# Optimization experiments

Hardware: AMD Instinct MI355X
Metric: run time of the kernel (lower is better)

## Reference

```python
import jax, jax.numpy as jnp
import numpy as np
from jax.ops import segment_sum


def gcn_conv(x, src, dst, W, b, num_nodes):
    # PyG GCNConv: x' = D^{-1/2} (A + I) D^{-1/2} (x @ W) + b
    loops = jnp.arange(num_nodes, dtype=src.dtype)
    s = jnp.concatenate([src, loops])  # source of each edge (incl. self-loops)
    d = jnp.concatenate([dst, loops])  # destination of each edge
    ones = jnp.ones(s.shape[0], dtype=x.dtype)
    deg = segment_sum(ones, d, num_segments=num_nodes)  # in-degree incl. self-loop
    dinv = jnp.where(deg > 0, jax.lax.rsqrt(deg), 0.0)
    norm = dinv[s] * dinv[d]  # [E+N]
    h = x @ W  # [N, C_out] dense transform first (C_out <= C_in typical)
    msg = h[s] * norm[:, None]  # gather + scale  [E+N, C_out]
    out = segment_sum(msg, d, num_segments=num_nodes)  # scatter-add
    return out + b


def setup_inputs() -> dict:
    key = jax.random.key(0)
    k1, k2, k3, k4 = jax.random.split(key, 4)
    N, E = 100000, 1600000
    C_in, C_out = 64, 32
    C_hid = 2 * C_out
    x = jax.random.normal(k1, (N, C_in), dtype=jnp.float32)
    edge_index = jax.random.randint(k2, (2, E), 0, N, dtype=jnp.int64)
    # Glorot-style init for the linear weights, zero bias (PyG defaults)
    W1 = jax.random.normal(k3, (C_in, C_hid), dtype=jnp.float32) * (1.0 / np.sqrt(C_in))
    b1 = jnp.zeros((C_hid,), dtype=jnp.float32)
    W2 = jax.random.normal(k4, (C_hid, C_out), dtype=jnp.float32) * (1.0 / np.sqrt(C_hid))
    b2 = jnp.zeros((C_out,), dtype=jnp.float32)
    return {"x": x, "edge_index": edge_index, "num_nodes": N,
            "W1": W1, "b1": b1, "W2": W2, "b2": b2}


def reference(x, edge_index, num_nodes, W1, b1, W2, b2):
    src, dst = edge_index[0], edge_index[1]
    h = gcn_conv(x, src, dst, W1, b1, num_nodes)
    h = jax.nn.relu(h)
    out = gcn_conv(h, src, dst, W2, b2, num_nodes)
    return out
```

## Files before the change

kernel.cpp:

```cpp
#include <hip/hip_runtime.h>


constexpr int CAP = 4096;
constexpr int NBMAX = 1024;
constexpr float QS = 2048.f;
constexpr float QSI = 1.f / 2048.f;

__device__ inline int sxlo(unsigned u) { return (int)(short)(u & 0xffffu); }
__device__ inline int sxhi(unsigned u) { return ((int)u) >> 16; }

__global__ __launch_bounds__(256) void p1_bin(const int* __restrict__ src,
                                              const int* __restrict__ dst,
                                              int* __restrict__ bucketCursor,
                                              unsigned* __restrict__ staging, int E, int NB) {
    __shared__ int cnt[NBMAX];
    __shared__ int cur[NBMAX];
    int tid = threadIdx.x;
    for (int i = tid; i < NB; i += 256) cnt[i] = 0;
    __syncthreads();
    int e0 = blockIdx.x * 4096;
#pragma unroll
    for (int k = 0; k < 16; ++k) {
        int e = e0 + k * 256 + tid;
        if (e < E) atomicAdd(&cnt[dst[e] >> 7], 1);
    }
    __syncthreads();
    for (int i = tid; i < NB; i += 256) {
        int c = cnt[i];
        cur[i] = c ? atomicAdd(&bucketCursor[i], c) : 0;
    }
    __syncthreads();
#pragma unroll
    for (int k = 0; k < 16; ++k) {
        int e = e0 + k * 256 + tid;
        if (e < E) {
            int d = dst[e];
            int b = d >> 7;
            int slot = atomicAdd(&cur[b], 1);
            staging[(size_t)b * CAP + slot] = ((unsigned)src[e] << 7) | (unsigned)(d & 127);
        }
    }
}

__global__ __launch_bounds__(256) void deg_dinv(const unsigned* __restrict__ staging,
                                                const int* __restrict__ bucketCursor,
                                                float* __restrict__ dinv, int N) {
    __shared__ int deg[128];
    int b = blockIdx.x, tid = threadIdx.x;
    if (tid < 128) deg[tid] = 0;
    __syncthreads();
    int size = bucketCursor[b];
    const unsigned* st = staging + (size_t)b * CAP;
    for (int i = tid; i < size; i += 256) atomicAdd(&deg[st[i] & 127u], 1);
    __syncthreads();
    int g = b * 128 + tid;
    if (tid < 128 && g < N) dinv[g] = rsqrtf((float)(deg[tid] + 1));
}

__global__ __launch_bounds__(256) void gemm1(const float* __restrict__ X,
                                             const float* __restrict__ W,
                                             const float* __restrict__ dinv,
                                             unsigned* __restrict__ Hout, int N) {
    constexpr int XS = 65;
    __shared__ float Xs[128 * XS];
    __shared__ float Ws[64 * 64];
    int tid = threadIdx.x;
    int rowBase = blockIdx.x * 128;
    const float4* Wv = (const float4*)W;
    float4* Wsv = (float4*)Ws;
    for (int i = tid; i < 64 * 64 / 4; i += 256) Wsv[i] = Wv[i];
    const float4* Xv = (const float4*)X;
    for (int v = tid; v < 128 * 16; v += 256) {
        int r = v >> 4, j = v & 15;
        int gr = rowBase + r;
        float4 t = make_float4(0.f, 0.f, 0.f, 0.f);
        if (gr < N) t = Xv[(size_t)gr * 16 + j];
        int b = r * XS + j * 4;
        Xs[b] = t.x;
        Xs[b + 1] = t.y;
        Xs[b + 2] = t.z;
        Xs[b + 3] = t.w;
    }
    __syncthreads();
    int cg = tid % 8, rg = tid / 8;
    int c0 = cg * 8, r0 = rg * 4;
    float acc[4][8];
#pragma unroll
    for (int i = 0; i < 4; ++i)
#pragma unroll
        for (int j = 0; j < 8; ++j) acc[i][j] = 0.f;
#pragma unroll 8
    for (int k = 0; k < 64; ++k) {
        float4 w0 = *(const float4*)&Ws[k * 64 + c0];
        float4 w1 = *(const float4*)&Ws[k * 64 + c0 + 4];
        float xr[4];
#pragma unroll
        for (int i = 0; i < 4; ++i) xr[i] = Xs[(r0 + i) * XS + k];
#pragma unroll
        for (int i = 0; i < 4; ++i) {
            acc[i][0] = fmaf(xr[i], w0.x, acc[i][0]);
            acc[i][1] = fmaf(xr[i], w0.y, acc[i][1]);
            acc[i][2] = fmaf(xr[i], w0.z, acc[i][2]);
            acc[i][3] = fmaf(xr[i], w0.w, acc[i][3]);
            acc[i][4] = fmaf(xr[i], w1.x, acc[i][4]);
            acc[i][5] = fmaf(xr[i], w1.y, acc[i][5]);
            acc[i][6] = fmaf(xr[i], w1.z, acc[i][6]);
            acc[i][7] = fmaf(xr[i], w1.w, acc[i][7]);
        }
    }
#pragma unroll
    for (int i = 0; i < 4; ++i) {
        int row = rowBase + r0 + i;
        if (row >= N) continue;
        float dq = dinv[row] * QS;
        unsigned pk[4];
#pragma unroll
        for (int j = 0; j < 4; ++j) {
            int lo = (int)(acc[i][2 * j] * dq);
            int hi = (int)(acc[i][2 * j + 1] * dq);
            pk[j] = ((unsigned)lo & 0xffffu) | ((unsigned)hi << 16);
        }
        *(uint4*)(Hout + (size_t)row * 32 + c0 / 2) = make_uint4(pk[0], pk[1], pk[2], pk[3]);
    }
}

__global__ __launch_bounds__(256) void agg1(const uint4* __restrict__ hs1,
                                            const unsigned* __restrict__ staging,
                                            const int* __restrict__ bucketCursor,
                                            const float* __restrict__ dinv,
                                            const float* __restrict__ b1,
                                            unsigned* __restrict__ a1, int N) {
    constexpr int S1 = 65;
    __shared__ int acc[128 * S1];
    __shared__ float b1s[64];
    int b = blockIdx.x, tid = threadIdx.x;
    int gbase = b * 128;
    if (tid < 64) b1s[tid] = QS * b1[tid];
    for (int v = tid; v < 128 * 8; v += 256) {
        int n = v >> 3, j = v & 7;
        int s0 = 0, s1 = 0, s2 = 0, s3 = 0, s4 = 0, s5 = 0, s6 = 0, s7 = 0;
        if (gbase + n < N) {
            uint4 u = hs1[(size_t)(gbase + n) * 8 + j];
            s0 = sxlo(u.x); s1 = sxhi(u.x);
            s2 = sxlo(u.y); s3 = sxhi(u.y);
            s4 = sxlo(u.z); s5 = sxhi(u.z);
            s6 = sxlo(u.w); s7 = sxhi(u.w);
        }
        int* dp = &acc[n * S1 + j * 8];
        dp[0] = s0; dp[1] = s1; dp[2] = s2; dp[3] = s3;
        dp[4] = s4; dp[5] = s5; dp[6] = s6; dp[7] = s7;
    }
    __syncthreads();
    int size = bucketCursor[b];
    const unsigned* st = staging + (size_t)b * CAP;
    int g = tid >> 3, q = tid & 7;
#define ADD8(NN, U)                          \
    {                                        \
        int* ap = &acc[(int)(NN) * S1 + q * 8]; \
        atomicAdd(ap + 0, sxlo((U).x));      \
        atomicAdd(ap + 1, sxhi((U).x));      \
        atomicAdd(ap + 2, sxlo((U).y));      \
        atomicAdd(ap + 3, sxhi((U).y));      \
        atomicAdd(ap + 4, sxlo((U).z));      \
        atomicAdd(ap + 5, sxhi((U).z));      \
        atomicAdd(ap + 6, sxlo((U).w));      \
        atomicAdd(ap + 7, sxhi((U).w));      \
    }
    int i = g;
    for (; i + 224 < size; i += 256) {
        unsigned w[8];
        uint4 u[8];
#pragma unroll
        for (int k = 0; k < 8; ++k) w[k] = st[i + 32 * k];
#pragma unroll
        for (int k = 0; k < 8; ++k) u[k] = hs1[(size_t)(w[k] >> 7) * 8 + q];
#pragma unroll
        for (int k = 0; k < 8; ++k) ADD8(w[k] & 127u, u[k])
    }
    for (; i < size; i += 32) {
        unsigned w = st[i];
        uint4 u = hs1[(size_t)(w >> 7) * 8 + q];
        ADD8(w & 127u, u)
    }
#undef ADD8
    __syncthreads();
    for (int v = tid; v < 128 * 32; v += 256) {
        int n = v >> 5, cc = (v & 31) * 2;
        int gn = gbase + n;
        if (gn >= N) continue;
        float dn = dinv[gn];
        float x0 = fmaxf(fmaf((float)acc[n * S1 + cc], dn, b1s[cc]), 0.f);
        float x1 = fmaxf(fmaf((float)acc[n * S1 + cc + 1], dn, b1s[cc + 1]), 0.f);
        int q0 = (int)x0, q1 = (int)x1;
        a1[(size_t)gn * 32 + (cc >> 1)] = ((unsigned)q0 & 0xffffu) | ((unsigned)q1 << 16);
    }
}

__global__ __launch_bounds__(256) void gemm2(const uint4* __restrict__ a1,
                                             const float* __restrict__ W2,
                                             const float* __restrict__ dinv,
                                             unsigned* __restrict__ h2, int N) {
    constexpr int XS = 65;
    __shared__ float Xs[128 * XS];
    __shared__ float Ws[64 * 32];
    int tid = threadIdx.x;
    int rowBase = blockIdx.x * 128;
    const float4* Wv = (const float4*)W2;
    float4* Wsv = (float4*)Ws;
    for (int i = tid; i < 64 * 32 / 4; i += 256) Wsv[i] = Wv[i];
    for (int v = tid; v < 128 * 8; v += 256) {
        int r = v >> 3, j = v & 7;
        int gr = rowBase + r;
        float f0 = 0.f, f1 = 0.f, f2 = 0.f, f3 = 0.f, f4 = 0.f, f5 = 0.f, f6 = 0.f, f7 = 0.f;
        if (gr < N) {
            uint4 u = a1[(size_t)gr * 8 + j];
            f0 = (float)sxlo(u.x); f1 = (float)sxhi(u.x);
            f2 = (float)sxlo(u.y); f3 = (float)sxhi(u.y);
            f4 = (float)sxlo(u.z); f5 = (float)sxhi(u.z);
            f6 = (float)sxlo(u.w); f7 = (float)sxhi(u.w);
        }
        float* dp = &Xs[r * XS + j * 8];
        dp[0] = f0; dp[1] = f1; dp[2] = f2; dp[3] = f3;
        dp[4] = f4; dp[5] = f5; dp[6] = f6; dp[7] = f7;
    }
    __syncthreads();
    int cg = tid & 3, rg = tid >> 2;
    int c0 = cg * 8, r0 = rg * 2;
    float acc[2][8];
#pragma unroll
    for (int i = 0; i < 2; ++i)
#pragma unroll
        for (int j = 0; j < 8; ++j) acc[i][j] = 0.f;
#pragma unroll 8
    for (int k = 0; k < 64; ++k) {
        float4 w0 = *(const float4*)&Ws[k * 32 + c0];
        float4 w1 = *(const float4*)&Ws[k * 32 + c0 + 4];
        float x0 = Xs[r0 * XS + k];
        float x1 = Xs[(r0 + 1) * XS + k];
        acc[0][0] = fmaf(x0, w0.x, acc[0][0]);
        acc[0][1] = fmaf(x0, w0.y, acc[0][1]);
        acc[0][2] = fmaf(x0, w0.z, acc[0][2]);
        acc[0][3] = fmaf(x0, w0.w, acc[0][3]);
        acc[0][4] = fmaf(x0, w1.x, acc[0][4]);
        acc[0][5] = fmaf(x0, w1.y, acc[0][5]);
        acc[0][6] = fmaf(x0, w1.z, acc[0][6]);
        acc[0][7] = fmaf(x0, w1.w, acc[0][7]);
        acc[1][0] = fmaf(x1, w0.x, acc[1][0]);
        acc[1][1] = fmaf(x1, w0.y, acc[1][1]);
        acc[1][2] = fmaf(x1, w0.z, acc[1][2]);
        acc[1][3] = fmaf(x1, w0.w, acc[1][3]);
        acc[1][4] = fmaf(x1, w1.x, acc[1][4]);
        acc[1][5] = fmaf(x1, w1.y, acc[1][5]);
        acc[1][6] = fmaf(x1, w1.z, acc[1][6]);
        acc[1][7] = fmaf(x1, w1.w, acc[1][7]);
    }
#pragma unroll
    for (int i = 0; i < 2; ++i) {
        int row = rowBase + r0 + i;
        if (row >= N) continue;
        float dn = dinv[row];
        unsigned pk[2];
#pragma unroll
        for (int j = 0; j < 2; ++j) {
            int lo = (int)(acc[i][4 * j + 0] * dn);
            int l1 = (int)(acc[i][4 * j + 1] * dn);
            int l2 = (int)(acc[i][4 * j + 2] * dn);
            int l3 = (int)(acc[i][4 * j + 3] * dn);
            pk[0] = ((unsigned)lo & 0xffffu) | ((unsigned)l1 << 16);
            pk[1] = ((unsigned)l2 & 0xffffu) | ((unsigned)l3 << 16);
            *(uint2*)(h2 + (size_t)row * 16 + (c0 + 4 * j) / 2) = make_uint2(pk[0], pk[1]);
        }
    }
}

__global__ __launch_bounds__(256) void agg2(const uint4* __restrict__ hs2,
                                            const unsigned* __restrict__ staging,
                                            const int* __restrict__ bucketCursor,
                                            const float* __restrict__ dinv,
                                            const float* __restrict__ b2,
                                            float* __restrict__ out, int N) {
    constexpr int S2 = 33;
    __shared__ int acc[128 * S2];
    __shared__ float b2s[32];
    int b = blockIdx.x, tid = threadIdx.x;
    int gbase = b * 128;
    if (tid < 32) b2s[tid] = b2[tid];
    for (int v = tid; v < 128 * 4; v += 256) {
        int n = v >> 2, j = v & 3;
        int s0 = 0, s1 = 0, s2 = 0, s3 = 0, s4 = 0, s5 = 0, s6 = 0, s7 = 0;
        if (gbase + n < N) {
            uint4 u = hs2[(size_t)(gbase + n) * 4 + j];
            s0 = sxlo(u.x); s1 = sxhi(u.x);
            s2 = sxlo(u.y); s3 = sxhi(u.y);
            s4 = sxlo(u.z); s5 = sxhi(u.z);
            s6 = sxlo(u.w); s7 = sxhi(u.w);
        }
        int* dp = &acc[n * S2 + j * 8];
        dp[0] = s0; dp[1] = s1; dp[2] = s2; dp[3] = s3;
        dp[4] = s4; dp[5] = s5; dp[6] = s6; dp[7] = s7;
    }
    __syncthreads();
    int size = bucketCursor[b];
    const unsigned* st = staging + (size_t)b * CAP;
    int g = tid >> 2, q = tid & 3;
#define ADD8(NN, U)                          \
    {                                        \
        int* ap = &acc[(int)(NN) * S2 + q * 8]; \
        atomicAdd(ap + 0, sxlo((U).x));      \
        atomicAdd(ap + 1, sxhi((U).x));      \
        atomicAdd(ap + 2, sxlo((U).y));      \
        atomicAdd(ap + 3, sxhi((U).y));      \
        atomicAdd(ap + 4, sxlo((U).z));      \
        atomicAdd(ap + 5, sxhi((U).z));      \
        atomicAdd(ap + 6, sxlo((U).w));      \
        atomicAdd(ap + 7, sxhi((U).w));      \
    }
    int i = g;
    for (; i + 448 < size; i += 512) {
        unsigned w[8];
        uint4 u[8];
#pragma unroll
        for (int k = 0; k < 8; ++k) w[k] = st[i + 64 * k];
#pragma unroll
        for (int k = 0; k < 8; ++k) u[k] = hs2[(size_t)(w[k] >> 7) * 4 + q];
#pragma unroll
        for (int k = 0; k < 8; ++k) ADD8(w[k] & 127u, u[k])
    }
    for (; i < size; i += 64) {
        unsigned w = st[i];
        uint4 u = hs2[(size_t)(w >> 7) * 4 + q];
        ADD8(w & 127u, u)
    }
#undef ADD8
    __syncthreads();
    for (int v = tid; v < 128 * 32; v += 256) {
        int n = v >> 5, c = v & 31;
        int gn = gbase + n;
        if (gn >= N) continue;
        out[(size_t)gn * 32 + c] = fmaf((float)acc[n * S2 + c], dinv[gn] * QSI, b2s[c]);
    }
}

extern "C" void kernel_launch(void* const* d_in, const int* in_sizes, int n_in,
                              void* d_out, int out_size, void* d_ws, size_t ws_size,
                              hipStream_t stream) {
    const float* x = (const float*)d_in[0];
    const int* ei = (const int*)d_in[1];
    const float* W1 = (const float*)d_in[3];
    const float* b1 = (const float*)d_in[4];
    const float* W2 = (const float*)d_in[5];
    const float* b2 = (const float*)d_in[6];

    constexpr int CIN = 64, CHID = 64, COUT = 32;
    const int N = in_sizes[0] / CIN;
    const int E = in_sizes[1] / 2;
    const int* src = ei;
    const int* dst = ei + E;
    const int NB = (N + 127) >> 7;

    char* p = (char*)d_ws;
    auto carve = [&](size_t bytes) -> void* {
        void* q = (void*)p;
        p += (bytes + 255) & ~(size_t)255;
        return q;
    };
    int* bucketCursor = (int*)carve((size_t)NB * 4);
    float* dinv = (float*)carve((size_t)N * 4);
    unsigned* staging = (unsigned*)carve((size_t)NB * CAP * 4);
    unsigned* h1 = (unsigned*)carve((size_t)N * CHID * 2);
    unsigned* a1 = (unsigned*)carve((size_t)N * CHID * 2);
    unsigned* h2 = (unsigned*)carve((size_t)N * COUT * 2);

    hipMemsetAsync(bucketCursor, 0, (size_t)NB * 4, stream);
    p1_bin<<<(E + 4095) / 4096, 256, 0, stream>>>(src, dst, bucketCursor, staging, E, NB);
    deg_dinv<<<NB, 256, 0, stream>>>(staging, bucketCursor, dinv, N);
    gemm1<<<(N + 127) / 128, 256, 0, stream>>>(x, W1, dinv, h1, N);
    agg1<<<NB, 256, 0, stream>>>((const uint4*)h1, staging, bucketCursor, dinv, b1, a1, N);
    gemm2<<<(N + 127) / 128, 256, 0, stream>>>((const uint4*)a1, W2, dinv, h2, N);
    agg2<<<NB, 256, 0, stream>>>((const uint4*)h2, staging, bucketCursor, dinv, b2,
                                 (float*)d_out, N);
}
```

Before: 218.1 us.

## Fuse degree count into binning and gemm2 into layer-1 aggregation

Degree counting moves into the binning kernel through global atomics on a per-node int array, so the separate deg_dinv kernel is removed and consumers compute rsqrt on the fly. The layer-1 aggregation kernel now applies bias and ReLU in shared memory and runs the 64x32 second GEMM directly, which drops the a1 intermediate round trip and a launch. The binning block size is halved to 2048 edges. In exchange this adds 1.6M global atomics on deg and more shared memory per aggregation block, which may lower occupancy. It also changes numerics, because the hidden activations no longer go through int16 quantization before the second GEMM.

```diff
diff --git a/kernel.cpp b/kernel.cpp
--- a/kernel.cpp
+++ b/kernel.cpp
@@ -12,17 +12,22 @@
 __global__ __launch_bounds__(256) void p1_bin(const int* __restrict__ src,
                                               const int* __restrict__ dst,
                                               int* __restrict__ bucketCursor,
+                                              int* __restrict__ deg,
                                               unsigned* __restrict__ staging, int E, int NB) {
     __shared__ int cnt[NBMAX];
     __shared__ int cur[NBMAX];
     int tid = threadIdx.x;
     for (int i = tid; i < NB; i += 256) cnt[i] = 0;
     __syncthreads();
-    int e0 = blockIdx.x * 4096;
-#pragma unroll
-    for (int k = 0; k < 16; ++k) {
+    int e0 = blockIdx.x * 2048;
+#pragma unroll
+    for (int k = 0; k < 8; ++k) {
         int e = e0 + k * 256 + tid;
-        if (e < E) atomicAdd(&cnt[dst[e] >> 7], 1);
+        if (e < E) {
+            int d = dst[e];
+            atomicAdd(&cnt[d >> 7], 1);
+            atomicAdd(&deg[d], 1);
+        }
     }
     __syncthreads();
     for (int i = tid; i < NB; i += 256) {
@@ -31,7 +36,7 @@
     }
     __syncthreads();
 #pragma unroll
-    for (int k = 0; k < 16; ++k) {
+    for (int k = 0; k < 8; ++k) {
         int e = e0 + k * 256 + tid;
         if (e < E) {
             int d = dst[e];
@@ -42,24 +47,9 @@
     }
 }
 
-__global__ __launch_bounds__(256) void deg_dinv(const unsigned* __restrict__ staging,
-                                                const int* __restrict__ bucketCursor,
-                                                float* __restrict__ dinv, int N) {
-    __shared__ int deg[128];
-    int b = blockIdx.x, tid = threadIdx.x;
-    if (tid < 128) deg[tid] = 0;
-    __syncthreads();
-    int size = bucketCursor[b];
-    const unsigned* st = staging + (size_t)b * CAP;
-    for (int i = tid; i < size; i += 256) atomicAdd(&deg[st[i] & 127u], 1);
-    __syncthreads();
-    int g = b * 128 + tid;
-    if (tid < 128 && g < N) dinv[g] = rsqrtf((float)(deg[tid] + 1));
-}
-
 __global__ __launch_bounds__(256) void gemm1(const float* __restrict__ X,
                                              const float* __restrict__ W,
-                                             const float* __restrict__ dinv,
+                                             const int* __restrict__ deg,
                                              unsigned* __restrict__ Hout, int N) {
     constexpr int XS = 65;
     __shared__ float Xs[128 * XS];
@@ -112,7 +102,7 @@
     for (int i = 0; i < 4; ++i) {
         int row = rowBase + r0 + i;
         if (row >= N) continue;
-        float dq = dinv[row] * QS;
+        float dq = rsqrtf((float)(deg[row] + 1)) * QS;
         unsigned pk[4];
 #pragma unroll
         for (int j = 0; j < 4; ++j) {
@@ -124,18 +114,26 @@
     }
 }
 
-__global__ __launch_bounds__(256) void agg1(const uint4* __restrict__ hs1,
-                                            const unsigned* __restrict__ staging,
-                                            const int* __restrict__ bucketCursor,
-                                            const float* __restrict__ dinv,
-                                            const float* __restrict__ b1,
-                                            unsigned* __restrict__ a1, int N) {
+__global__ __launch_bounds__(256) void agg1_gemm2(
+    const uint4* __restrict__ hs1, const unsigned* __restrict__ staging,
+    const int* __restrict__ bucketCursor, const int* __restrict__ deg,
+    const float* __restrict__ b1, const float* __restrict__ W2,
+    unsigned* __restrict__ h2, int N) {
     constexpr int S1 = 65;
     __shared__ int acc[128 * S1];
+    __shared__ float Ws[64 * 32];
     __shared__ float b1s[64];
+    __shared__ float dns[128];
     int b = blockIdx.x, tid = threadIdx.x;
     int gbase = b * 128;
+    const float4* Wv = (const float4*)W2;
+    float4* Wsv = (float4*)Ws;
+    for (int i = tid; i < 64 * 32 / 4; i += 256) Wsv[i] = Wv[i];
     if (tid < 64) b1s[tid] = QS * b1[tid];
+    if (tid < 128) {
+        int gn = gbase + tid;
+        dns[tid] = (gn < N) ? rsqrtf((float)(deg[gn] + 1)) : 0.f;
+    }
     for (int v = tid; v < 128 * 8; v += 256) {
         int n = v >> 3, j = v & 7;
         int s0 = 0, s1 = 0, s2 = 0, s3 = 0, s4 = 0, s5 = 0, s6 = 0, s7 = 0;
@@ -154,17 +152,17 @@
     int size = bucketCursor[b];
     const unsigned* st = staging + (size_t)b * CAP;
     int g = tid >> 3, q = tid & 7;
-#define ADD8(NN, U)                          \
-    {                                        \
+#define ADD8(NN, U)                             \
+    {                                           \
         int* ap = &acc[(int)(NN) * S1 + q * 8]; \
-        atomicAdd(ap + 0, sxlo((U).x));      \
-        atomicAdd(ap + 1, sxhi((U).x));      \
-        atomicAdd(ap + 2, sxlo((U).y));      \
-        atomicAdd(ap + 3, sxhi((U).y));      \
-        atomicAdd(ap + 4, sxlo((U).z));      \
-        atomicAdd(ap + 5, sxhi((U).z));      \
-        atomicAdd(ap + 6, sxlo((U).w));      \
-        atomicAdd(ap + 7, sxhi((U).w));      \
+        atomicAdd(ap + 0, sxlo((U).x));         \
+        atomicAdd(ap + 1, sxhi((U).x));         \
+        atomicAdd(ap + 2, sxlo((U).y));         \
+        atomicAdd(ap + 3, sxhi((U).y));         \
+        atomicAdd(ap + 4, sxlo((U).z));         \
+        atomicAdd(ap + 5, sxhi((U).z));         \
+        atomicAdd(ap + 6, sxlo((U).w));         \
+        atomicAdd(ap + 7, sxhi((U).w));         \
     }
     int i = g;
     for (; i + 224 < size; i += 256) {
@@ -184,99 +182,62 @@
     }
 #undef ADD8
     __syncthreads();
-    for (int v = tid; v < 128 * 32; v += 256) {
-        int n = v >> 5, cc = (v & 31) * 2;
-        int gn = gbase + n;
-        if (gn >= N) continue;
-        float dn = dinv[gn];
-        float x0 = fmaxf(fmaf((float)acc[n * S1 + cc], dn, b1s[cc]), 0.f);
-        float x1 = fmaxf(fmaf((float)acc[n * S1 + cc + 1], dn, b1s[cc + 1]), 0.f);
-        int q0 = (int)x0, q1 = (int)x1;
-        a1[(size_t)gn * 32 + (cc >> 1)] = ((unsigned)q0 & 0xffffu) | ((unsigned)q1 << 16);
-    }
-}
-
-__global__ __launch_bounds__(256) void gemm2(const uint4* __restrict__ a1,
-                                             const float* __restrict__ W2,
-                                             const float* __restrict__ dinv,
-                                             unsigned* __restrict__ h2, int N) {
-    constexpr int XS = 65;
-    __shared__ float Xs[128 * XS];
-    __shared__ float Ws[64 * 32];
-    int tid = threadIdx.x;
-    int rowBase = blockIdx.x * 128;
-    const float4* Wv = (const float4*)W2;
-    float4* Wsv = (float4*)Ws;
-    for (int i = tid; i < 64 * 32 / 4; i += 256) Wsv[i] = Wv[i];
-    for (int v = tid; v < 128 * 8; v += 256) {
-        int r = v >> 3, j = v & 7;
-        int gr = rowBase + r;
-        float f0 = 0.f, f1 = 0.f, f2 = 0.f, f3 = 0.f, f4 = 0.f, f5 = 0.f, f6 = 0.f, f7 = 0.f;
-        if (gr < N) {
-            uint4 u = a1[(size_t)gr * 8 + j];
-            f0 = (float)sxlo(u.x); f1 = (float)sxhi(u.x);
-            f2 = (float)sxlo(u.y); f3 = (float)sxhi(u.y);
-            f4 = (float)sxlo(u.z); f5 = (float)sxhi(u.z);
-            f6 = (float)sxlo(u.w); f7 = (float)sxhi(u.w);
-        }
-        float* dp = &Xs[r * XS + j * 8];
-        dp[0] = f0; dp[1] = f1; dp[2] = f2; dp[3] = f3;
-        dp[4] = f4; dp[5] = f5; dp[6] = f6; dp[7] = f7;
+    float* af = (float*)acc;
+    for (int v = tid; v < 128 * 64; v += 256) {
+        int n = v >> 6, c = v & 63;
+        af[n * S1 + c] = fmaxf(fmaf((float)acc[n * S1 + c], dns[n], b1s[c]), 0.f);
     }
     __syncthreads();
     int cg = tid & 3, rg = tid >> 2;
     int c0 = cg * 8, r0 = rg * 2;
-    float acc[2][8];
-#pragma unroll
-    for (int i = 0; i < 2; ++i)
-#pragma unroll
-        for (int j = 0; j < 8; ++j) acc[i][j] = 0.f;
+    float a2[2][8];
+#pragma unroll
+    for (int i2 = 0; i2 < 2; ++i2)
+#pragma unroll
+        for (int j = 0; j < 8; ++j) a2[i2][j] = 0.f;
 #pragma unroll 8
     for (int k = 0; k < 64; ++k) {
         float4 w0 = *(const float4*)&Ws[k * 32 + c0];
         float4 w1 = *(const float4*)&Ws[k * 32 + c0 + 4];
-        float x0 = Xs[r0 * XS + k];
-        float x1 = Xs[(r0 + 1) * XS + k];
-        acc[0][0] = fmaf(x0, w0.x, acc[0][0]);
-        acc[0][1] = fmaf(x0, w0.y, acc[0][1]);
-        acc[0][2] = fmaf(x0, w0.z, acc[0][2]);
-        acc[0][3] = fmaf(x0, w0.w, acc[0][3]);
-        acc[0][4] = fmaf(x0, w1.x, acc[0][4]);
-        acc[0][5] = fmaf(x0, w1.y, acc[0][5]);
-        acc[0][6] = fmaf(x0, w1.z, acc[0][6]);
-        acc[0][7] = fmaf(x0, w1.w, acc[0][7]);
-        acc[1][0] = fmaf(x1, w0.x, acc[1][0]);
-        acc[1][1] = fmaf(x1, w0.y, acc[1][1]);
-        acc[1][2] = fmaf(x1, w0.z, acc[1][2]);
-        acc[1][3] = fmaf(x1, w0.w, acc[1][3]);
-        acc[1][4] = fmaf(x1, w1.x, acc[1][4]);
-        acc[1][5] = fmaf(x1, w1.y, acc[1][5]);
-        acc[1][6] = fmaf(x1, w1.z, acc[1][6]);
-        acc[1][7] = fmaf(x1, w1.w, acc[1][7]);
-    }
-#pragma unroll
-    for (int i = 0; i < 2; ++i) {
-        int row = rowBase + r0 + i;
+        float x0 = af[r0 * S1 + k];
+        float x1 = af[(r0 + 1) * S1 + k];
+        a2[0][0] = fmaf(x0, w0.x, a2[0][0]);
+        a2[0][1] = fmaf(x0, w0.y, a2[0][1]);
+        a2[0][2] = fmaf(x0, w0.z, a2[0][2]);
+        a2[0][3] = fmaf(x0, w0.w, a2[0][3]);
+        a2[0][4] = fmaf(x0, w1.x, a2[0][4]);
+        a2[0][5] = fmaf(x0, w1.y, a2[0][5]);
+        a2[0][6] = fmaf(x0, w1.z, a2[0][6]);
+        a2[0][7] = fmaf(x0, w1.w, a2[0][7]);
+        a2[1][0] = fmaf(x1, w0.x, a2[1][0]);
+        a2[1][1] = fmaf(x1, w0.y, a2[1][1]);
+        a2[1][2] = fmaf(x1, w0.z, a2[1][2]);
+        a2[1][3] = fmaf(x1, w0.w, a2[1][3]);
+        a2[1][4] = fmaf(x1, w1.x, a2[1][4]);
+        a2[1][5] = fmaf(x1, w1.y, a2[1][5]);
+        a2[1][6] = fmaf(x1, w1.z, a2[1][6]);
+        a2[1][7] = fmaf(x1, w1.w, a2[1][7]);
+    }
+#pragma unroll
+    for (int i2 = 0; i2 < 2; ++i2) {
+        int row = gbase + r0 + i2;
         if (row >= N) continue;
-        float dn = dinv[row];
-        unsigned pk[2];
-#pragma unroll
-        for (int j = 0; j < 2; ++j) {
-            int lo = (int)(acc[i][4 * j + 0] * dn);
-            int l1 = (int)(acc[i][4 * j + 1] * dn);
-            int l2 = (int)(acc[i][4 * j + 2] * dn);
-            int l3 = (int)(acc[i][4 * j + 3] * dn);
-            pk[0] = ((unsigned)lo & 0xffffu) | ((unsigned)l1 << 16);
-            pk[1] = ((unsigned)l2 & 0xffffu) | ((unsigned)l3 << 16);
-            *(uint2*)(h2 + (size_t)row * 16 + (c0 + 4 * j) / 2) = make_uint2(pk[0], pk[1]);
-        }
+        float dn = dns[r0 + i2];
+        unsigned pk[4];
+#pragma unroll
+        for (int j = 0; j < 4; ++j) {
+            int lo = (int)(a2[i2][2 * j] * dn);
+            int hi = (int)(a2[i2][2 * j + 1] * dn);
+            pk[j] = ((unsigned)lo & 0xffffu) | ((unsigned)hi << 16);
+        }
+        *(uint4*)(h2 + (size_t)row * 16 + c0 / 2) = make_uint4(pk[0], pk[1], pk[2], pk[3]);
     }
 }
 
 __global__ __launch_bounds__(256) void agg2(const uint4* __restrict__ hs2,
                                             const unsigned* __restrict__ staging,
                                             const int* __restrict__ bucketCursor,
-                                            const float* __restrict__ dinv,
+                                            const int* __restrict__ deg,
                                             const float* __restrict__ b2,
                                             float* __restrict__ out, int N) {
     constexpr int S2 = 33;
@@ -303,17 +264,17 @@
     int size = bucketCursor[b];
     const unsigned* st = staging + (size_t)b * CAP;
     int g = tid >> 2, q = tid & 3;
-#define ADD8(NN, U)                          \
-    {                                        \
+#define ADD8(NN, U)                             \
+    {                                           \
         int* ap = &acc[(int)(NN) * S2 + q * 8]; \
-        atomicAdd(ap + 0, sxlo((U).x));      \
-        atomicAdd(ap + 1, sxhi((U).x));      \
-        atomicAdd(ap + 2, sxlo((U).y));      \
-        atomicAdd(ap + 3, sxhi((U).y));      \
-        atomicAdd(ap + 4, sxlo((U).z));      \
-        atomicAdd(ap + 5, sxhi((U).z));      \
-        atomicAdd(ap + 6, sxlo((U).w));      \
-        atomicAdd(ap + 7, sxhi((U).w));      \
+        atomicAdd(ap + 0, sxlo((U).x));         \
+        atomicAdd(ap + 1, sxhi((U).x));         \
+        atomicAdd(ap + 2, sxlo((U).y));         \
+        atomicAdd(ap + 3, sxhi((U).y));         \
+        atomicAdd(ap + 4, sxlo((U).z));         \
+        atomicAdd(ap + 5, sxhi((U).z));         \
+        atomicAdd(ap + 6, sxlo((U).w));         \
+        atomicAdd(ap + 7, sxhi((U).w));         \
     }
     int i = g;
     for (; i + 448 < size; i += 512) {
@@ -337,7 +298,8 @@
         int n = v >> 5, c = v & 31;
         int gn = gbase + n;
         if (gn >= N) continue;
-        out[(size_t)gn * 32 + c] = fmaf((float)acc[n * S2 + c], dinv[gn] * QSI, b2s[c]);
+        float dn = rsqrtf((float)(deg[gn] + 1));
+        out[(size_t)gn * 32 + c] = fmaf((float)acc[n * S2 + c], dn * QSI, b2s[c]);
     }
 }
 
@@ -365,18 +327,17 @@
         return q;
     };
     int* bucketCursor = (int*)carve((size_t)NB * 4);
-    float* dinv = (float*)carve((size_t)N * 4);
+    int* deg = (int*)carve((size_t)N * 4);
     unsigned* staging = (unsigned*)carve((size_t)NB * CAP * 4);
     unsigned* h1 = (unsigned*)carve((size_t)N * CHID * 2);
-    unsigned* a1 = (unsigned*)carve((size_t)N * CHID * 2);
     unsigned* h2 = (unsigned*)carve((size_t)N * COUT * 2);
 
-    hipMemsetAsync(bucketCursor, 0, (size_t)NB * 4, stream);
-    p1_bin<<<(E + 4095) / 4096, 256, 0, stream>>>(src, dst, bucketCursor, staging, E, NB);
-    deg_dinv<<<NB, 256, 0, stream>>>(staging, bucketCursor, dinv, N);
-    gemm1<<<(N + 127) / 128, 256, 0, stream>>>(x, W1, dinv, h1, N);
-    agg1<<<NB, 256, 0, stream>>>((const uint4*)h1, staging, bucketCursor, dinv, b1, a1, N);
-    gemm2<<<(N + 127) / 128, 256, 0, stream>>>((const uint4*)a1, W2, dinv, h2, N);
-    agg2<<<NB, 256, 0, stream>>>((const uint4*)h2, staging, bucketCursor, dinv, b2,
+    size_t zbytes = (size_t)((char*)(deg + N) - (char*)bucketCursor);
+    hipMemsetAsync(bucketCursor, 0, zbytes, stream);
+    p1_bin<<<(E + 2047) / 2048, 256, 0, stream>>>(src, dst, bucketCursor, deg, staging, E, NB);
+    gemm1<<<(N + 127) / 128, 256, 0, stream>>>(x, W1, deg, h1, N);
+    agg1_gemm2<<<NB, 256, 0, stream>>>((const uint4*)h1, staging, bucketCursor, deg, b1, W2,
+                                       h2, N);
+    agg2<<<NB, 256, 0, stream>>>((const uint4*)h2, staging, bucketCursor, deg, b2,
                                  (float*)d_out, N);
 }
```

New measurement: 275.6 us. 26.4% more time.
